# Optimization experiments

Hardware: AMD Instinct MI355X
Metric: run time of the kernel (lower is better)

## Reference

```python
import jax, jax.numpy as jnp
import numpy as np

B, N, P, K, C = 8, 4096, 4096, 32, 128  # batch, points, npoint, neighbors, channels (=mlp[-1])
W_OUT = 16  # weightnet output channels (from Linear(16*mlp[-1], mlp[-1]))
EPS = 1e-5


def setup_inputs() -> dict:
    key = jax.random.key(0)
    ks = jax.random.split(key, 9)
    xyz = jax.random.normal(ks[0], (B, P, 3), jnp.float32)
    points = jax.random.normal(ks[1], (B, N, C), jnp.float32)
    local_coordinates = jax.random.normal(ks[2], (B, P, K, 3), jnp.float32)
    neighbor_lists = jax.random.randint(ks[3], (B, P, K), 0, N)
    data_idx = jax.random.randint(ks[4], (B,), 0, B)
    Ww = jax.random.normal(ks[5], (3, W_OUT), jnp.float32) * 0.1   # weightnet (pointwise linear 3->16)
    bw = jnp.zeros((W_OUT,), jnp.float32)
    Wl = jax.random.normal(ks[6], (W_OUT * C, C), jnp.float32) * 0.02  # nn.Linear(16*mlp[-1], mlp[-1])
    bl = jnp.zeros((C,), jnp.float32)
    gamma = jnp.ones((C,), jnp.float32)   # BatchNorm1d weight
    beta = jnp.zeros((C,), jnp.float32)   # BatchNorm1d bias
    return {"xyz": xyz, "points": points, "local_coordinates": local_coordinates,
            "neighbor_lists": neighbor_lists, "data_idx": data_idx,
            "Ww": Ww, "bw": bw, "Wl": Wl, "bl": bl, "gamma": gamma, "beta": beta}


def reference(xyz, points, local_coordinates, neighbor_lists, data_idx, Ww, bw, Wl, bl, gamma, beta):
    b, p, k, _ = local_coordinates.shape
    c = points.shape[-1]
    # weightnet: pointwise map of 3-D local coordinates to 16 weight channels -> [B,P,K,16]
    weights = local_coordinates @ Ww + bw
    # irregular neighbor gather: data[b,p,k,:] = points[b, neighbor_lists[b,p,k], :] -> [B,P,K,C]
    data = points[jnp.arange(b)[:, None, None], neighbor_lists]
    # per-point weighted aggregation over K neighbors: [B,P,C,16] -> flatten to [B,P,C*16]
    new_points = jnp.einsum('bpkc,bpkw->bpcw', data, weights).reshape(b, p, c * weights.shape[-1])
    # batch reindex via data_idx
    new_points = new_points[data_idx]
    # linear tail: [B,P,C]
    new_points = new_points @ Wl + bl
    # BatchNorm1d over channel dim (training-mode batch stats), then ReLU: [B,C,P]
    x = new_points.transpose(0, 2, 1)
    mean = x.mean(axis=(0, 2), keepdims=True)
    var = x.var(axis=(0, 2), keepdims=True)
    x = (x - mean) * jax.lax.rsqrt(var + EPS) * gamma[None, :, None] + beta[None, :, None]
    return xyz, jax.nn.relu(x)
```

## Files before the change

kernel.cpp:

```cpp
#include <hip/hip_runtime.h>

#define Bn 8
#define Nn 4096
#define Pn 4096
#define Kn 32
#define Cn 128

using float4v = __attribute__((ext_vector_type(4))) float;
using short8  = __attribute__((ext_vector_type(8))) short;

__device__ __forceinline__ unsigned short bf16b(float f) {
  union { float f; unsigned u; } v; v.f = f;
  unsigned r = v.u + 0x7FFFu + ((v.u >> 16) & 1u);
  return (unsigned short)(r >> 16);
}

__device__ __forceinline__ unsigned pkhi(float x, float y) {
  return __builtin_amdgcn_perm(__float_as_uint(y), __float_as_uint(x), 0x07060302u);
}

__device__ __forceinline__ void gld_lds16(const void* g, void* l) {
  __builtin_amdgcn_global_load_lds(
      (const __attribute__((address_space(1))) unsigned int*)g,
      (__attribute__((address_space(3))) unsigned int*)l, 16, 0, 0);
}

__global__ __launch_bounds__(256) void prep(const float* __restrict__ Wl,
                                            unsigned short* __restrict__ WlT,
                                            const float* __restrict__ xyz,
                                            float* __restrict__ out,
                                            float* __restrict__ gacc) {
  __shared__ unsigned short tile[128 * 130];
  const int t = threadIdx.x, blk = blockIdx.x;
  if (blk < 16) {
#pragma unroll
    for (int i = 0; i < 64; ++i) {
      int idx = i * 256 + t;
      int kl = idx >> 7, n = idx & 127;
      tile[n * 130 + kl] = bf16b(Wl[(size_t)(blk * 128 + kl) * 128 + n]);
    }
    __syncthreads();
#pragma unroll
    for (int i = 0; i < 64; ++i) {
      int idx = i * 256 + t;
      int n = idx >> 7, kl = idx & 127;
      WlT[(size_t)n * 2048 + blk * 128 + kl] = tile[n * 130 + kl];
    }
  } else {
    if (blk == 16) gacc[t] = 0.f;
    const int i0 = (blk - 16) * 3072 + t * 12;
#pragma unroll
    for (int i = 0; i < 3; ++i)
      *(float4v*)(out + i0 + i * 4) = *(const float4v*)(xyz + i0 + i * 4);
  }
}

__global__ __launch_bounds__(64) void stage1(
    const float* __restrict__ points, const float* __restrict__ lc,
    const int* __restrict__ nl, const int* __restrict__ didx,
    const float* __restrict__ Ww, const float* __restrict__ bwv,
    unsigned short* __restrict__ Mglob) {
  __shared__ unsigned short slab[32 * 128];

  const int lane = threadIdx.x;
  const int l15 = lane & 15, q = lane >> 4;
  const int b = blockIdx.x & 7;
  const int pg = blockIdx.x >> 3;
  const int db = didx[b];
  const float2* __restrict__ pbat2 =
      (const float2*)(points + (size_t)db * Nn * Cn);
  const float Ww0 = Ww[l15], Ww1 = Ww[16 + l15], Ww2 = Ww[32 + l15];
  const float bw0 = bwv[l15];

  for (int pi = 0; pi < 4; ++pi) {
    const int p = pg * 4 + pi;
    const unsigned pk = (unsigned)((db * Pn + p) * Kn);
    int nk[32];
    const int4* __restrict__ nl4 = (const int4*)(nl + pk);
#pragma unroll
    for (int i = 0; i < 8; ++i) *(int4*)&nk[i * 4] = nl4[i];
    const float* __restrict__ lcp = lc + (size_t)(pk + q * 8) * 3;
    float la[24];
#pragma unroll
    for (int v = 0; v < 6; ++v) *(float4v*)&la[v * 4] = *(const float4v*)(lcp + v * 4);
    short8 af;
#pragma unroll
    for (int j = 0; j < 8; ++j) {
      float w = bw0 + la[3 * j] * Ww0 + la[3 * j + 1] * Ww1 + la[3 * j + 2] * Ww2;
      af[j] = (short)bf16b(w);
    }
    __builtin_amdgcn_wave_barrier();
#pragma unroll
    for (int r = 0; r < 32; ++r) {
      const float2 v = pbat2[((unsigned)nk[r] << 6) + lane];
      const unsigned idx = r * 128 + ((lane * 2 + (r >> 3) * 16) & 127);
      *(unsigned*)&slab[idx] = pkhi(v.x, v.y);
    }
    __builtin_amdgcn_wave_barrier();
    const unsigned moff = ((unsigned)(b * Pn + p)) << 11;
#pragma unroll
    for (int ct = 0; ct < 8; ++ct) {
      const int coff = (ct * 16 + l15 + q * 16) & 127;
      short8 bfv;
#pragma unroll
      for (int j = 0; j < 8; ++j)
        bfv[j] = (short)slab[(q * 8 + j) * 128 + coff];
      float4v d = {0.f, 0.f, 0.f, 0.f};
      d = __builtin_amdgcn_mfma_f32_16x16x32_bf16(af, bfv, d, 0, 0, 0);
      uint2 u;
      u.x = pkhi(d[0], d[1]);
      u.y = pkhi(d[2], d[3]);
      *(uint2*)&Mglob[moff + (ct * 16 + l15) * 16 + q * 4] = u;
    }
    __builtin_amdgcn_wave_barrier();
  }
}

__global__ __launch_bounds__(256) void stage2(
    const unsigned short* __restrict__ Mglob,
    const unsigned short* __restrict__ WlT, const float* __restrict__ blv,
    float* __restrict__ xout, float* __restrict__ gacc) {
  __shared__ unsigned short As[32 * 64];
  __shared__ unsigned short Bs[128 * 64];
  __shared__ float red[256];

  const int t = threadIdx.x, lane = t & 63, wave = t >> 6;
  const int l15 = lane & 15, q = lane >> 4;
  const int lr = lane >> 3, lchk = lane & 7;
  const int bidx = blockIdx.x & 7;
  const int pt0 = (blockIdx.x >> 3) * 32;
  const size_t row0 = (size_t)bidx * Pn + pt0;

  float4v acc[2][2];
#pragma unroll
  for (int rt = 0; rt < 2; ++rt)
#pragma unroll
    for (int nt = 0; nt < 2; ++nt) acc[rt][nt] = (float4v){0.f, 0.f, 0.f, 0.f};

  for (int kk = 0; kk < 32; ++kk) {
    const int k0 = kk * 64;
    gld_lds16(Mglob + (row0 + wave * 8 + lr) * 2048 + k0 + (lchk ^ lr) * 8,
              &As[wave * 8 * 64]);
#pragma unroll
    for (int it = 0; it < 4; ++it) {
      const int n = wave * 32 + it * 8 + lr;
      gld_lds16(WlT + (size_t)n * 2048 + k0 + (lchk ^ lr) * 8,
                &Bs[(wave * 32 + it * 8) * 64]);
    }
    __syncthreads();
#pragma unroll
    for (int ks = 0; ks < 2; ++ks) {
      short8 a[2], bq[2];
#pragma unroll
      for (int rt = 0; rt < 2; ++rt) {
        const int row = rt * 16 + l15;
        a[rt] = *(const short8*)&As[row * 64 + (((ks * 4 + q) ^ (row & 7)) << 3)];
      }
#pragma unroll
      for (int nt = 0; nt < 2; ++nt) {
        const int n = wave * 32 + nt * 16 + l15;
        bq[nt] = *(const short8*)&Bs[n * 64 + (((ks * 4 + q) ^ (n & 7)) << 3)];
      }
#pragma unroll
      for (int rt = 0; rt < 2; ++rt)
#pragma unroll
        for (int nt = 0; nt < 2; ++nt)
          acc[rt][nt] = __builtin_amdgcn_mfma_f32_16x16x32_bf16(a[rt], bq[nt],
                                                                acc[rt][nt], 0, 0, 0);
    }
    __syncthreads();
  }

#pragma unroll
  for (int nt = 0; nt < 2; ++nt) {
    const int ch = wave * 32 + nt * 16 + l15;
    const float bb = blv[ch];
    float s = 0.f, sq = 0.f;
#pragma unroll
    for (int rt = 0; rt < 2; ++rt) {
      float4v o;
#pragma unroll
      for (int r = 0; r < 4; ++r) {
        float v = acc[rt][nt][r] + bb; o[r] = v; s += v; sq += v * v;
      }
      *(float4v*)(xout + ((size_t)bidx * Cn + ch) * Pn + pt0 + rt * 16 + q * 4) = o;
    }
    s += __shfl_xor(s, 16); s += __shfl_xor(s, 32);
    sq += __shfl_xor(sq, 16); sq += __shfl_xor(sq, 32);
    if (lane < 16) { red[ch] = s; red[128 + ch] = sq; }
  }
  __syncthreads();
  atomicAdd(&gacc[t], red[t]);
}

__global__ __launch_bounds__(256) void finalize_ln(float* __restrict__ x,
                                                   const float* __restrict__ gacc,
                                                   const float* __restrict__ gamma,
                                                   const float* __restrict__ beta) {
  const int idx = blockIdx.x * 256 + threadIdx.x;
  const int fi = idx * 4;
  const int c = (fi >> 12) & 127;
  const float inv = 1.f / 32768.f;
  const float mean = gacc[c] * inv;
  const float var = gacc[128 + c] * inv - mean * mean;
  const float scale = rsqrtf(var + 1e-5f) * gamma[c];
  const float shift = beta[c] - mean * scale;
  float4v v = *(float4v*)(x + fi);
#pragma unroll
  for (int r = 0; r < 4; ++r) v[r] = fmaxf(v[r] * scale + shift, 0.f);
  *(float4v*)(x + fi) = v;
}

extern "C" void kernel_launch(void* const* d_in, const int* in_sizes, int n_in,
                              void* d_out, int out_size, void* d_ws, size_t ws_size,
                              hipStream_t stream) {
  const float* xyz    = (const float*)d_in[0];
  const float* points = (const float*)d_in[1];
  const float* lc     = (const float*)d_in[2];
  const int*   nl     = (const int*)d_in[3];
  const int*   didx   = (const int*)d_in[4];
  const float* Ww     = (const float*)d_in[5];
  const float* bw     = (const float*)d_in[6];
  const float* Wl     = (const float*)d_in[7];
  const float* bl     = (const float*)d_in[8];
  const float* gamma  = (const float*)d_in[9];
  const float* beta   = (const float*)d_in[10];

  float* out  = (float*)d_out;
  float* xout = out + (size_t)Bn * Pn * 3;
  unsigned short* WlT = (unsigned short*)d_ws;
  float* gacc = (float*)((char*)d_ws + (size_t)512 * 1024);
  unsigned short* Mglob =
      (unsigned short*)((char*)d_ws + (size_t)1024 * 1024);

  prep<<<48, 256, 0, stream>>>(Wl, WlT, xyz, out, gacc);
  stage1<<<8192, 64, 0, stream>>>(points, lc, nl, didx, Ww, bw, Mglob);
  stage2<<<1024, 256, 0, stream>>>(Mglob, WlT, bl, xout, gacc);
  finalize_ln<<<4096, 256, 0, stream>>>(xout, gacc, gamma, beta);
}
```

Measured before the change: 215.9 us.

## Gather neighbor features directly into MFMA registers and drop LDS staging in both stages

Stage1 now loads each lane's MFMA B-operand fragment straight from the gathered point rows into registers, removing the LDS slab, and packs four points per 256-thread block. Stage2 drops the LDS tiles and global_load_lds, loading A and B fragments directly from global memory with a register double-buffer and a 64-row tile per block. The aim is to avoid LDS round-trips and block-wide barriers. In exchange, gather loads become 4-byte scattered accesses, register pressure rises, and stage2 loses shared-memory reuse of WlT across waves.

```diff
diff --git a/kernel.cpp b/kernel.cpp
--- a/kernel.cpp
+++ b/kernel.cpp
@@ -17,12 +17,6 @@
 
 __device__ __forceinline__ unsigned pkhi(float x, float y) {
   return __builtin_amdgcn_perm(__float_as_uint(y), __float_as_uint(x), 0x07060302u);
-}
-
-__device__ __forceinline__ void gld_lds16(const void* g, void* l) {
-  __builtin_amdgcn_global_load_lds(
-      (const __attribute__((address_space(1))) unsigned int*)g,
-      (__attribute__((address_space(3))) unsigned int*)l, 16, 0, 0);
 }
 
 __global__ __launch_bounds__(256) void prep(const float* __restrict__ Wl,
@@ -55,30 +49,32 @@
   }
 }
 
-__global__ __launch_bounds__(64) void stage1(
+__global__ __launch_bounds__(256, 3) void stage1(
     const float* __restrict__ points, const float* __restrict__ lc,
     const int* __restrict__ nl, const int* __restrict__ didx,
     const float* __restrict__ Ww, const float* __restrict__ bwv,
     unsigned short* __restrict__ Mglob) {
-  __shared__ unsigned short slab[32 * 128];
-
-  const int lane = threadIdx.x;
+  const int t = threadIdx.x;
+  const int lane = t & 63, wv = t >> 6;
   const int l15 = lane & 15, q = lane >> 4;
   const int b = blockIdx.x & 7;
   const int pg = blockIdx.x >> 3;
   const int db = didx[b];
-  const float2* __restrict__ pbat2 =
-      (const float2*)(points + (size_t)db * Nn * Cn);
+  const char* __restrict__ pbase = (const char*)(points + (size_t)db * Nn * Cn);
   const float Ww0 = Ww[l15], Ww1 = Ww[16 + l15], Ww2 = Ww[32 + l15];
   const float bw0 = bwv[l15];
 
+  const int p0 = pg * 16 + wv * 4;
+#pragma unroll 1
   for (int pi = 0; pi < 4; ++pi) {
-    const int p = pg * 4 + pi;
+    const int p = p0 + pi;
     const unsigned pk = (unsigned)((db * Pn + p) * Kn);
-    int nk[32];
-    const int4* __restrict__ nl4 = (const int4*)(nl + pk);
-#pragma unroll
-    for (int i = 0; i < 8; ++i) *(int4*)&nk[i * 4] = nl4[i];
+
+    int nk[8];
+    const int4* __restrict__ nlq = (const int4*)(nl + pk + q * 8);
+    *(int4*)&nk[0] = nlq[0];
+    *(int4*)&nk[4] = nlq[1];
+
     const float* __restrict__ lcp = lc + (size_t)(pk + q * 8) * 3;
     float la[24];
 #pragma unroll
@@ -89,30 +85,33 @@
       float w = bw0 + la[3 * j] * Ww0 + la[3 * j + 1] * Ww1 + la[3 * j + 2] * Ww2;
       af[j] = (short)bf16b(w);
     }
-    __builtin_amdgcn_wave_barrier();
-#pragma unroll
-    for (int r = 0; r < 32; ++r) {
-      const float2 v = pbat2[((unsigned)nk[r] << 6) + lane];
-      const unsigned idx = r * 128 + ((lane * 2 + (r >> 3) * 16) & 127);
-      *(unsigned*)&slab[idx] = pkhi(v.x, v.y);
-    }
-    __builtin_amdgcn_wave_barrier();
+
+    unsigned base[8];
+#pragma unroll
+    for (int j = 0; j < 8; ++j)
+      base[j] = ((unsigned)nk[j] << 9) + (unsigned)(l15 * 4);
+
+    float f[64];
+#pragma unroll
+    for (int ct = 0; ct < 8; ++ct)
+#pragma unroll
+      for (int j = 0; j < 8; ++j)
+        f[ct * 8 + j] = *(const float*)(pbase + base[j] + ct * 64);
+
     const unsigned moff = ((unsigned)(b * Pn + p)) << 11;
 #pragma unroll
     for (int ct = 0; ct < 8; ++ct) {
-      const int coff = (ct * 16 + l15 + q * 16) & 127;
-      short8 bfv;
-#pragma unroll
-      for (int j = 0; j < 8; ++j)
-        bfv[j] = (short)slab[(q * 8 + j) * 128 + coff];
+      union { short8 s; unsigned u[4]; } bv;
+#pragma unroll
+      for (int i = 0; i < 4; ++i)
+        bv.u[i] = pkhi(f[ct * 8 + 2 * i], f[ct * 8 + 2 * i + 1]);
       float4v d = {0.f, 0.f, 0.f, 0.f};
-      d = __builtin_amdgcn_mfma_f32_16x16x32_bf16(af, bfv, d, 0, 0, 0);
+      d = __builtin_amdgcn_mfma_f32_16x16x32_bf16(af, bv.s, d, 0, 0, 0);
       uint2 u;
       u.x = pkhi(d[0], d[1]);
       u.y = pkhi(d[2], d[3]);
       *(uint2*)&Mglob[moff + (ct * 16 + l15) * 16 + q * 4] = u;
     }
-    __builtin_amdgcn_wave_barrier();
   }
 }
 
@@ -120,56 +119,57 @@
     const unsigned short* __restrict__ Mglob,
     const unsigned short* __restrict__ WlT, const float* __restrict__ blv,
     float* __restrict__ xout, float* __restrict__ gacc) {
-  __shared__ unsigned short As[32 * 64];
-  __shared__ unsigned short Bs[128 * 64];
   __shared__ float red[256];
-
   const int t = threadIdx.x, lane = t & 63, wave = t >> 6;
   const int l15 = lane & 15, q = lane >> 4;
-  const int lr = lane >> 3, lchk = lane & 7;
   const int bidx = blockIdx.x & 7;
-  const int pt0 = (blockIdx.x >> 3) * 32;
+  const int pt0 = (blockIdx.x >> 3) * 64;
   const size_t row0 = (size_t)bidx * Pn + pt0;
 
-  float4v acc[2][2];
-#pragma unroll
-  for (int rt = 0; rt < 2; ++rt)
+  const unsigned short* __restrict__ ap = Mglob + (row0 + l15) * 2048 + q * 8;
+  const unsigned short* __restrict__ bp =
+      WlT + (size_t)(wave * 32 + l15) * 2048 + q * 8;
+
+  float4v acc[4][2];
+#pragma unroll
+  for (int rt = 0; rt < 4; ++rt)
 #pragma unroll
     for (int nt = 0; nt < 2; ++nt) acc[rt][nt] = (float4v){0.f, 0.f, 0.f, 0.f};
 
-  for (int kk = 0; kk < 32; ++kk) {
-    const int k0 = kk * 64;
-    gld_lds16(Mglob + (row0 + wave * 8 + lr) * 2048 + k0 + (lchk ^ lr) * 8,
-              &As[wave * 8 * 64]);
-#pragma unroll
-    for (int it = 0; it < 4; ++it) {
-      const int n = wave * 32 + it * 8 + lr;
-      gld_lds16(WlT + (size_t)n * 2048 + k0 + (lchk ^ lr) * 8,
-                &Bs[(wave * 32 + it * 8) * 64]);
-    }
-    __syncthreads();
-#pragma unroll
-    for (int ks = 0; ks < 2; ++ks) {
-      short8 a[2], bq[2];
-#pragma unroll
-      for (int rt = 0; rt < 2; ++rt) {
-        const int row = rt * 16 + l15;
-        a[rt] = *(const short8*)&As[row * 64 + (((ks * 4 + q) ^ (row & 7)) << 3)];
-      }
-#pragma unroll
-      for (int nt = 0; nt < 2; ++nt) {
-        const int n = wave * 32 + nt * 16 + l15;
-        bq[nt] = *(const short8*)&Bs[n * 64 + (((ks * 4 + q) ^ (n & 7)) << 3)];
-      }
-#pragma unroll
-      for (int rt = 0; rt < 2; ++rt)
-#pragma unroll
-        for (int nt = 0; nt < 2; ++nt)
-          acc[rt][nt] = __builtin_amdgcn_mfma_f32_16x16x32_bf16(a[rt], bq[nt],
-                                                                acc[rt][nt], 0, 0, 0);
-    }
-    __syncthreads();
-  }
+  short8 aA[4], bA[2], aB[4], bB[2];
+
+#define LDA(buf, kk)                                              \
+  buf[0] = *(const short8*)(ap + (kk) * 32);                      \
+  buf[1] = *(const short8*)(ap + 32768 + (kk) * 32);              \
+  buf[2] = *(const short8*)(ap + 65536 + (kk) * 32);              \
+  buf[3] = *(const short8*)(ap + 98304 + (kk) * 32);
+#define LDB(buf, kk)                                              \
+  buf[0] = *(const short8*)(bp + (kk) * 32);                      \
+  buf[1] = *(const short8*)(bp + 32768 + (kk) * 32);
+#define CMP(ab, bb)                                                                  \
+  acc[0][0] = __builtin_amdgcn_mfma_f32_16x16x32_bf16(ab[0], bb[0], acc[0][0], 0, 0, 0); \
+  acc[0][1] = __builtin_amdgcn_mfma_f32_16x16x32_bf16(ab[0], bb[1], acc[0][1], 0, 0, 0); \
+  acc[1][0] = __builtin_amdgcn_mfma_f32_16x16x32_bf16(ab[1], bb[0], acc[1][0], 0, 0, 0); \
+  acc[1][1] = __builtin_amdgcn_mfma_f32_16x16x32_bf16(ab[1], bb[1], acc[1][1], 0, 0, 0); \
+  acc[2][0] = __builtin_amdgcn_mfma_f32_16x16x32_bf16(ab[2], bb[0], acc[2][0], 0, 0, 0); \
+  acc[2][1] = __builtin_amdgcn_mfma_f32_16x16x32_bf16(ab[2], bb[1], acc[2][1], 0, 0, 0); \
+  acc[3][0] = __builtin_amdgcn_mfma_f32_16x16x32_bf16(ab[3], bb[0], acc[3][0], 0, 0, 0); \
+  acc[3][1] = __builtin_amdgcn_mfma_f32_16x16x32_bf16(ab[3], bb[1], acc[3][1], 0, 0, 0);
+
+  LDA(aA, 0) LDB(bA, 0)
+#pragma unroll 1
+  for (int kk = 0; kk < 62; kk += 2) {
+    LDA(aB, kk + 1) LDB(bB, kk + 1)
+    CMP(aA, bA)
+    LDA(aA, kk + 2) LDB(bA, kk + 2)
+    CMP(aB, bB)
+  }
+  LDA(aB, 63) LDB(bB, 63)
+  CMP(aA, bA)
+  CMP(aB, bB)
+#undef LDA
+#undef LDB
+#undef CMP
 
 #pragma unroll
   for (int nt = 0; nt < 2; ++nt) {
@@ -177,7 +177,7 @@
     const float bb = blv[ch];
     float s = 0.f, sq = 0.f;
 #pragma unroll
-    for (int rt = 0; rt < 2; ++rt) {
+    for (int rt = 0; rt < 4; ++rt) {
       float4v o;
 #pragma unroll
       for (int r = 0; r < 4; ++r) {
@@ -234,7 +234,7 @@
       (unsigned short*)((char*)d_ws + (size_t)1024 * 1024);
 
   prep<<<48, 256, 0, stream>>>(Wl, WlT, xyz, out, gacc);
-  stage1<<<8192, 64, 0, stream>>>(points, lc, nl, didx, Ww, bw, Mglob);
-  stage2<<<1024, 256, 0, stream>>>(Mglob, WlT, bl, xout, gacc);
+  stage1<<<2048, 256, 0, stream>>>(points, lc, nl, didx, Ww, bw, Mglob);
+  stage2<<<512, 256, 0, stream>>>(Mglob, WlT, bl, xout, gacc);
   finalize_ln<<<4096, 256, 0, stream>>>(xout, gacc, gamma, beta);
 }
```

Measured after the change: 253.4 us. 17.3% more time.
